# Optimization experiments

Hardware: AMD Instinct MI355X
Metric: run time of the kernel (lower is better)

Reference implementation:

```python
import jax, jax.numpy as jnp
import numpy as np

B, S, LQ = 32, 1024, 128
EMB = 256; H = 256; NH = 8; DH = H // NH
NCATE, NCONT, NNODE = 4, 8, 4
VOCAB = 50000
EPS = 1e-5
LK = S - LQ


def _ln(x, g, b):
    mu = jnp.mean(x, -1, keepdims=True)
    xc = x - mu
    var = jnp.mean(xc * xc, -1, keepdims=True)
    return xc * jax.lax.rsqrt(var + EPS) * g + b


def _leaky(x):
    return jnp.where(x >= 0, x, 0.01 * x)  # LeakyReLU slope 0.01 (torch default)


def setup_inputs() -> dict:
    key = jax.random.key(0)
    ks = jax.random.split(key, 48)
    rnd = lambda i, shape, scale=0.02: jax.random.normal(ks[i], shape, dtype=jnp.float32) * scale
    rng = np.random.default_rng(0)
    qidx = jnp.asarray(np.sort(rng.choice(S, LQ, replace=False)).astype(np.int64))
    cate_table = rnd(6, (VOCAB, EMB)).at[0].set(0.0)  # padding_idx=0
    inp = {
        "node": jax.random.normal(ks[0], (B, S, EMB * NNODE), dtype=jnp.float32),
        "cate": jax.random.randint(ks[1], (B, S, NCATE), 0, VOCAB),
        "cont": jax.random.normal(ks[2], (B, S, NCONT), dtype=jnp.float32),
        "query_index": qidx,
        "mask": jax.random.bernoulli(ks[3], 0.1, (B, LK)),
        "cate_table": cate_table,
        "pos_emb": rnd(4, (1, S, H)),
        "node_W": rnd(5, (EMB * NNODE, H)), "node_b": jnp.zeros((H,), jnp.float32),
        "node_ln_g": jnp.ones((H,), jnp.float32), "node_ln_b": jnp.zeros((H,), jnp.float32),
        "cate_W": rnd(7, (EMB * NCATE, H)), "cate_b": jnp.zeros((H,), jnp.float32),
        "cate_ln_g": jnp.ones((H,), jnp.float32), "cate_ln_b": jnp.zeros((H,), jnp.float32),
        "bn_g": jnp.ones((NCONT,), jnp.float32), "bn_b": jnp.zeros((NCONT,), jnp.float32),
        "cont_W": rnd(8, (NCONT, H)), "cont_b": jnp.zeros((H,), jnp.float32),
        "cont_ln_g": jnp.ones((H,), jnp.float32), "cont_ln_b": jnp.zeros((H,), jnp.float32),
        "comb_W": rnd(9, (3 * H, H)), "comb_b": jnp.zeros((H,), jnp.float32),
        "comb_ln_g": jnp.ones((H,), jnp.float32), "comb_ln_b": jnp.zeros((H,), jnp.float32),
        "q_W": rnd(10, (H, H)), "q_b": jnp.zeros((H,), jnp.float32),
        "k_W": rnd(11, (H, H)), "k_b": jnp.zeros((H,), jnp.float32),
        "v_W": rnd(12, (H, H)), "v_b": jnp.zeros((H,), jnp.float32),
        "reg_W1": rnd(13, (H, H)), "reg_b1": jnp.zeros((H,), jnp.float32),
        "reg_ln_g": jnp.ones((H,), jnp.float32), "reg_ln_b": jnp.zeros((H,), jnp.float32),
        "reg_W2": rnd(14, (H, H)), "reg_b2": jnp.zeros((H,), jnp.float32),
    }
    return inp


def reference(node, cate, cont, query_index, mask, cate_table, pos_emb,
              node_W, node_b, node_ln_g, node_ln_b,
              cate_W, cate_b, cate_ln_g, cate_ln_b,
              bn_g, bn_b, cont_W, cont_b, cont_ln_g, cont_ln_b,
              comb_W, comb_b, comb_ln_g, comb_ln_b,
              q_W, q_b, k_W, k_b, v_W, v_b,
              reg_W1, reg_b1, reg_ln_g, reg_ln_b, reg_W2, reg_b2):
    # --- three embedding branches: Linear -> LayerNorm ---
    node_e = _ln(node @ node_W + node_b, node_ln_g, node_ln_b)
    ce = cate_table[cate].reshape(B, S, NCATE * EMB)  # embedding gather
    cate_e = _ln(ce @ cate_W + cate_b, cate_ln_g, cate_ln_b)
    # BatchNorm1d (training-mode batch stats, biased var) over flattened [B*S, C]
    cf = cont.reshape(-1, NCONT)
    mu = jnp.mean(cf, 0)
    var = jnp.mean((cf - mu) ** 2, 0)
    cn = ((cf - mu) * jax.lax.rsqrt(var + EPS) * bn_g + bn_b).reshape(B, S, NCONT)
    cont_e = _ln(cn @ cont_W + cont_b, cont_ln_g, cont_ln_b)
    # --- combine + positions ---
    seq = jnp.concatenate([node_e, cate_e, cont_e], -1)       # [B,S,3H]
    seq = _ln(_leaky(seq) @ comb_W + comb_b, comb_ln_g, comb_ln_b) + pos_emb  # [B,S,H]
    # --- gather-split cross attention: queries vs complement keys ---
    is_q = jnp.zeros((S,), bool).at[query_index].set(True)
    key_index = jnp.nonzero(~is_q, size=LK)[0]                # setdiff1d, static size
    q = seq[:, query_index]                                   # [B,LQ,H]
    kv = seq[:, key_index]                                    # [B,LK,H]
    Q = (q @ q_W + q_b).reshape(B, LQ, NH, DH).transpose(0, 2, 1, 3)
    K = (kv @ k_W + k_b).reshape(B, LK, NH, DH).transpose(0, 2, 1, 3)
    V = (kv @ v_W + v_b).reshape(B, LK, NH, DH).transpose(0, 2, 1, 3)
    scale = jnp.float32(1.0 / np.sqrt(DH))
    scores = jnp.einsum('bhqd,bhkd->bhqk', Q, K) * scale      # [B,NH,LQ,LK]
    scores = jnp.where(mask[:, None, None, :], jnp.float32(-1e9), scores)
    attn = jax.nn.softmax(scores, -1)                         # dropout = identity (eval)
    out = jnp.einsum('bhqk,bhkd->bhqd', attn, V).transpose(0, 2, 1, 3).reshape(B, LQ, H)
    h = _leaky(_ln(out @ reg_W1 + reg_b1, reg_ln_g, reg_ln_b))
    return h @ reg_W2 + reg_b2                                # [B,LQ,H]
```

## Files before the change

### kernel.cpp

```cpp
#include <hip/hip_runtime.h>
#include <cstdint>

#define EPSV 1e-5f
#define AS1 __attribute__((address_space(1)))
#define AS3 __attribute__((address_space(3)))

typedef __attribute__((ext_vector_type(8))) short short8v;
typedef __attribute__((ext_vector_type(4))) float float4v;

__device__ inline unsigned short f2bf(float f) {
    union { float f; unsigned int u; } v; v.f = f;
    unsigned int r = v.u + 0x7FFF + ((v.u >> 16) & 1);
    return (unsigned short)(r >> 16);
}

__device__ inline size_t bidx(int n, int k) {
    return ((size_t)(k >> 5) << 13) + ((size_t)(n >> 4) << 9)
         + (((k >> 3) & 3) << 7) + ((n & 15) << 3) + (k & 7);
}

__device__ inline void issue_b(const unsigned short* Bc, int s, unsigned short* bsb,
                               int w, int l) {
    const unsigned short* g = Bc + ((size_t)s << 13) + (w << 9) + (l << 3);
    unsigned short* d = bsb + (w << 9) + (l << 3);
    #pragma unroll
    for (int i = 0; i < 4; ++i)
        __builtin_amdgcn_global_load_lds((const AS1 void*)(g + (i << 11)),
                                         (AS3 void*)(d + (i << 11)), 16, 0, 0);
}

__global__ __launch_bounds__(256) void wt_all_k(
    const float* __restrict__ nW, const float* __restrict__ cW, const float* __restrict__ mW,
    const float* __restrict__ qW, const float* __restrict__ kW, const float* __restrict__ vW,
    const float* __restrict__ r1W, const float* __restrict__ r2W,
    unsigned short* __restrict__ nO, unsigned short* __restrict__ cO, unsigned short* __restrict__ mO,
    unsigned short* __restrict__ qO, unsigned short* __restrict__ kO, unsigned short* __restrict__ vO,
    unsigned short* __restrict__ r1O, unsigned short* __restrict__ r2O)
{
    __shared__ float T[64][65];
    int bid = blockIdx.x;
    const float* W; unsigned short* O; int K, tile;
    if (bid < 64)       { W = nW; O = nO; K = 1024; tile = bid; }
    else if (bid < 128) { W = cW; O = cO; K = 1024; tile = bid - 64; }
    else if (bid < 176) { W = mW; O = mO; K = 768;  tile = bid - 128; }
    else {
        int s = (bid - 176) >> 4; tile = (bid - 176) & 15; K = 256;
        switch (s) {
            case 0: W = qW;  O = qO;  break;
            case 1: W = kW;  O = kO;  break;
            case 2: W = vW;  O = vO;  break;
            case 3: W = r1W; O = r1O; break;
            default: W = r2W; O = r2O; break;
        }
    }
    int kTiles = K >> 6;
    int k0 = (tile % kTiles) * 64, n0 = (tile / kTiles) * 64;
    int c = threadIdx.x & 63, r4 = threadIdx.x >> 6;
    #pragma unroll
    for (int rr = 0; rr < 64; rr += 4) {
        int r = rr + r4;
        T[r][c] = W[(size_t)(k0 + r) * 256 + n0 + c];
    }
    __syncthreads();
    #pragma unroll
    for (int rr = 0; rr < 64; rr += 4) {
        int n = rr + r4;
        O[bidx(n0 + n, k0 + c)] = f2bf(T[c][n]);
    }
}

__global__ __launch_bounds__(256) void gemm_nc_k(
    const float* __restrict__ node, const int* __restrict__ cate,
    const float* __restrict__ table,
    const unsigned short* __restrict__ nWt, const unsigned short* __restrict__ cWt,
    const float* __restrict__ nb, const float* __restrict__ cb,
    const float* __restrict__ nlg, const float* __restrict__ nlb,
    const float* __restrict__ clg, const float* __restrict__ clb,
    unsigned short* __restrict__ Y)
{
    __shared__ unsigned short As[2][64][40];
    __shared__ unsigned short Bs[2][8192];
    __shared__ float redS[64][4], redQ[64][4];
    const int t = threadIdx.x;
    const bool isC = blockIdx.x >= 512;
    const int bm = (isC ? (int)blockIdx.x - 512 : (int)blockIdx.x) * 64;
    const int w = t >> 6, l = t & 63, lr = l & 15, lg = l >> 4;
    const int arow = t >> 2, ac8 = (t & 3) * 8;

    const unsigned short* Bc = isC ? cWt : nWt;
    const float* bias = isC ? cb : nb;
    const float* lng  = isC ? clg : nlg;
    const float* lnbp = isC ? clb : nlb;
    const int colOff = isC ? 256 : 0;

    const float* apf = node + (size_t)(bm + arow) * 1024 + ac8;
    int4 idx4 = {0,0,0,0};
    if (isC) idx4 = *(const int4*)&cate[(bm + arow) * 4];

    float4v acc[4][4];
    #pragma unroll
    for (int i = 0; i < 4; ++i)
        #pragma unroll
        for (int j = 0; j < 4; ++j) acc[i][j] = (float4v)0.f;

    float4 fA0, fA1, fB0, fB1;

    auto loadA = [&](int s, float4& f0, float4& f1) {
        int kt = s * 32;
        const float* p;
        if (isC) {
            int g = kt >> 8;
            int idx = (g == 0) ? idx4.x : (g == 1) ? idx4.y : (g == 2) ? idx4.z : idx4.w;
            p = table + (size_t)idx * 256 + (kt & 255) + ac8;
        } else {
            p = apf + kt;
        }
        f0 = *(const float4*)p;
        f1 = *(const float4*)(p + 4);
    };
    auto writeA = [&](const float4& f0, const float4& f1, unsigned short (*Asb)[40]) {
        short8v av;
        av[0] = (short)f2bf(f0.x); av[1] = (short)f2bf(f0.y);
        av[2] = (short)f2bf(f0.z); av[3] = (short)f2bf(f0.w);
        av[4] = (short)f2bf(f1.x); av[5] = (short)f2bf(f1.y);
        av[6] = (short)f2bf(f1.z); av[7] = (short)f2bf(f1.w);
        *(short8v*)&Asb[arow][ac8] = av;
    };
    auto comp = [&](unsigned short (*Asb)[40], unsigned short* bsb) {
        short8v af[4], bf[4];
        #pragma unroll
        for (int i = 0; i < 4; ++i) af[i] = *(const short8v*)&Asb[i*16 + lr][lg*8];
        #pragma unroll
        for (int j = 0; j < 4; ++j)
            bf[j] = *(const short8v*)&bsb[((w*4 + j) << 9) + (lg << 7) + (lr << 3)];
        #pragma unroll
        for (int i = 0; i < 4; ++i)
            #pragma unroll
            for (int j = 0; j < 4; ++j)
                acc[i][j] = __builtin_amdgcn_mfma_f32_16x16x32_bf16(af[i], bf[j], acc[i][j], 0, 0, 0);
    };

    issue_b(Bc, 0, &Bs[0][0], w, l);
    loadA(0, fA0, fA1);
    for (int s = 0; s < 32; ++s) {
        int cur = s & 1;
        __syncthreads();
        writeA(fA0, fA1, As[cur]);
        __syncthreads();
        if (s + 1 < 32) {
            issue_b(Bc, s + 1, &Bs[1 - cur][0], w, l);
            loadA(s + 1, fB0, fB1);
        }
        comp(As[cur], &Bs[cur][0]);
        fA0 = fB0; fA1 = fB1;
    }

    float bv[4];
    #pragma unroll
    for (int j = 0; j < 4; ++j) bv[j] = bias[w*64 + j*16 + lr];
    #pragma unroll
    for (int i = 0; i < 4; ++i)
        #pragma unroll
        for (int j = 0; j < 4; ++j)
            #pragma unroll
            for (int r4 = 0; r4 < 4; ++r4) acc[i][j][r4] += bv[j];

    float ps[4][4], qs[4][4];
    #pragma unroll
    for (int i = 0; i < 4; ++i)
        #pragma unroll
        for (int r4 = 0; r4 < 4; ++r4) {
            float a0 = acc[i][0][r4], a1 = acc[i][1][r4],
                  a2 = acc[i][2][r4], a3 = acc[i][3][r4];
            ps[i][r4] = (a0 + a1) + (a2 + a3);
            qs[i][r4] = (a0*a0 + a1*a1) + (a2*a2 + a3*a3);
        }
    #pragma unroll
    for (int o = 1; o < 16; o <<= 1)
        #pragma unroll
        for (int i = 0; i < 4; ++i)
            #pragma unroll
            for (int r4 = 0; r4 < 4; ++r4) {
                ps[i][r4] += __shfl_xor(ps[i][r4], o);
                qs[i][r4] += __shfl_xor(qs[i][r4], o);
            }
    if (lr == 0) {
        #pragma unroll
        for (int i = 0; i < 4; ++i)
            #pragma unroll
            for (int r4 = 0; r4 < 4; ++r4) {
                redS[i*16 + lg*4 + r4][w] = ps[i][r4];
                redQ[i*16 + lg*4 + r4][w] = qs[i][r4];
            }
    }
    __syncthreads();
    #pragma unroll
    for (int i = 0; i < 4; ++i) {
        float mu[4], rstd[4];
        #pragma unroll
        for (int r4 = 0; r4 < 4; ++r4) {
            int rl = i*16 + lg*4 + r4;
            float s  = (redS[rl][0] + redS[rl][1]) + (redS[rl][2] + redS[rl][3]);
            float qq = (redQ[rl][0] + redQ[rl][1]) + (redQ[rl][2] + redQ[rl][3]);
            float m_ = s * (1.0f/256.0f);
            mu[r4] = m_;
            rstd[r4] = rsqrtf(qq * (1.0f/256.0f) - m_*m_ + EPSV);
        }
        #pragma unroll
        for (int j = 0; j < 4; ++j) {
            int c = w*64 + j*16 + lr;
            float gv = lng[c], b2 = lnbp[c];
            #pragma unroll
            for (int r4 = 0; r4 < 4; ++r4) {
                int row = bm + i*16 + lg*4 + r4;
                float y = (acc[i][j][r4] - mu[r4]) * rstd[r4] * gv + b2;
                y = (y >= 0.f) ? y : 0.01f*y;
                Y[(size_t)row * 768 + colOff + c] = f2bf(y);
            }
        }
    }
}

__global__ __launch_bounds__(256) void gemm_comb_k(
    const unsigned short* __restrict__ A,
    const unsigned short* __restrict__ Bc,
    const float* __restrict__ bias,
    const float* __restrict__ lng, const float* __restrict__ lnbp,
    const float* __restrict__ pos,
    unsigned short* __restrict__ Y)
{
    __shared__ unsigned short As[2][32][40];
    __shared__ unsigned short Bs[2][8192];
    __shared__ float redS[32][4], redQ[32][4];
    const int t = threadIdx.x;
    const int bm = blockIdx.x * 32;
    const int w = t >> 6, l = t & 63, lr = l & 15, lg = l >> 4;
    const int arow = (t & 127) >> 2;
    const int ac8  = (t & 3) * 8;
    const bool aLane = t < 128;

    const unsigned short* ap = A + (size_t)(bm + arow) * 768 + ac8;

    float4v acc[2][4];
    #pragma unroll
    for (int i = 0; i < 2; ++i)
        #pragma unroll
        for (int j = 0; j < 4; ++j) acc[i][j] = (float4v)0.f;

    short8v aA, aB;

    auto comp = [&](unsigned short (*Asb)[40], unsigned short* bsb) {
        short8v af[2], bf[4];
        #pragma unroll
        for (int i = 0; i < 2; ++i) af[i] = *(const short8v*)&Asb[i*16 + lr][lg*8];
        #pragma unroll
        for (int j = 0; j < 4; ++j)
            bf[j] = *(const short8v*)&bsb[((w*4 + j) << 9) + (lg << 7) + (lr << 3)];
        #pragma unroll
        for (int i = 0; i < 2; ++i)
            #pragma unroll
            for (int j = 0; j < 4; ++j)
                acc[i][j] = __builtin_amdgcn_mfma_f32_16x16x32_bf16(af[i], bf[j], acc[i][j], 0, 0, 0);
    };

    issue_b(Bc, 0, &Bs[0][0], w, l);
    if (aLane) aA = *(const short8v*)(ap);
    for (int s = 0; s < 24; ++s) {
        int cur = s & 1;
        __syncthreads();
        if (aLane) *(short8v*)&As[cur][arow][ac8] = aA;
        __syncthreads();
        if (s + 1 < 24) {
            issue_b(Bc, s + 1, &Bs[1 - cur][0], w, l);
            if (aLane) aB = *(const short8v*)(ap + (s + 1) * 32);
        }
        comp(As[cur], &Bs[cur][0]);
        aA = aB;
    }

    float bv[4];
    #pragma unroll
    for (int j = 0; j < 4; ++j) bv[j] = bias[w*64 + j*16 + lr];
    #pragma unroll
    for (int i = 0; i < 2; ++i)
        #pragma unroll
        for (int j = 0; j < 4; ++j)
            #pragma unroll
            for (int r4 = 0; r4 < 4; ++r4) acc[i][j][r4] += bv[j];

    float ps[2][4], qs[2][4];
    #pragma unroll
    for (int i = 0; i < 2; ++i)
        #pragma unroll
        for (int r4 = 0; r4 < 4; ++r4) {
            float a0 = acc[i][0][r4], a1 = acc[i][1][r4],
                  a2 = acc[i][2][r4], a3 = acc[i][3][r4];
            ps[i][r4] = (a0 + a1) + (a2 + a3);
            qs[i][r4] = (a0*a0 + a1*a1) + (a2*a2 + a3*a3);
        }
    #pragma unroll
    for (int o = 1; o < 16; o <<= 1)
        #pragma unroll
        for (int i = 0; i < 2; ++i)
            #pragma unroll
            for (int r4 = 0; r4 < 4; ++r4) {
                ps[i][r4] += __shfl_xor(ps[i][r4], o);
                qs[i][r4] += __shfl_xor(qs[i][r4], o);
            }
    if (lr == 0) {
        #pragma unroll
        for (int i = 0; i < 2; ++i)
            #pragma unroll
            for (int r4 = 0; r4 < 4; ++r4) {
                redS[i*16 + lg*4 + r4][w] = ps[i][r4];
                redQ[i*16 + lg*4 + r4][w] = qs[i][r4];
            }
    }
    __syncthreads();
    #pragma unroll
    for (int i = 0; i < 2; ++i) {
        float mu[4], rstd[4];
        #pragma unroll
        for (int r4 = 0; r4 < 4; ++r4) {
            int rl = i*16 + lg*4 + r4;
            float s  = (redS[rl][0] + redS[rl][1]) + (redS[rl][2] + redS[rl][3]);
            float qq = (redQ[rl][0] + redQ[rl][1]) + (redQ[rl][2] + redQ[rl][3]);
            float m_ = s * (1.0f/256.0f);
            mu[r4] = m_;
            rstd[r4] = rsqrtf(qq * (1.0f/256.0f) - m_*m_ + EPSV);
        }
        #pragma unroll
        for (int j = 0; j < 4; ++j) {
            int c = w*64 + j*16 + lr;
            float gv = lng[c], b2 = lnbp[c];
            #pragma unroll
            for (int r4 = 0; r4 < 4; ++r4) {
                int row = bm + i*16 + lg*4 + r4;
                float y = (acc[i][j][r4] - mu[r4]) * rstd[r4] * gv + b2
                        + pos[(size_t)(row & 1023) * 256 + c];
                Y[(size_t)row * 256 + c] = f2bf(y);
            }
        }
    }
}

__global__ __launch_bounds__(256) void gemm_qkv_k(
    const unsigned short* __restrict__ seq,
    const int* __restrict__ qmap, const int* __restrict__ krmap,
    const unsigned short* __restrict__ qWt, const unsigned short* __restrict__ kWt,
    const unsigned short* __restrict__ vWt,
    const float* __restrict__ qb, const float* __restrict__ kb, const float* __restrict__ vb,
    unsigned short* __restrict__ Qo, unsigned short* __restrict__ Ko,
    unsigned short* __restrict__ Vt)
{
    __shared__ unsigned short As[2][64][40];
    __shared__ unsigned short Bs[2][8192];
    const int t = threadIdx.x;
    const int bid = blockIdx.x;
    int seg, bm;
    const int* gmap; const unsigned short* Bc; const float* bias;
    if (bid < 64)       { seg = 0; bm = bid * 64;         gmap = qmap;  Bc = qWt; bias = qb; }
    else if (bid < 512) { seg = 1; bm = (bid - 64) * 64;  gmap = krmap; Bc = kWt; bias = kb; }
    else                { seg = 2; bm = (bid - 512) * 64; gmap = krmap; Bc = vWt; bias = vb; }
    const int w = t >> 6, l = t & 63, lr = l & 15, lg = l >> 4;
    const int arow = t >> 2, ac8 = (t & 3) * 8;

    const unsigned short* ap = seq + (size_t)gmap[bm + arow] * 256 + ac8;

    float4v acc[4][4];
    #pragma unroll
    for (int i = 0; i < 4; ++i)
        #pragma unroll
        for (int j = 0; j < 4; ++j) acc[i][j] = (float4v)0.f;

    short8v aA, aB;

    auto comp = [&](unsigned short (*Asb)[40], unsigned short* bsb) {
        short8v af[4], bf[4];
        #pragma unroll
        for (int i = 0; i < 4; ++i) af[i] = *(const short8v*)&Asb[i*16 + lr][lg*8];
        #pragma unroll
        for (int j = 0; j < 4; ++j)
            bf[j] = *(const short8v*)&bsb[((w*4 + j) << 9) + (lg << 7) + (lr << 3)];
        #pragma unroll
        for (int i = 0; i < 4; ++i)
            #pragma unroll
            for (int j = 0; j < 4; ++j)
                acc[i][j] = __builtin_amdgcn_mfma_f32_16x16x32_bf16(af[i], bf[j], acc[i][j], 0, 0, 0);
    };

    issue_b(Bc, 0, &Bs[0][0], w, l);
    aA = *(const short8v*)(ap);
    for (int s = 0; s < 8; ++s) {
        int cur = s & 1;
        __syncthreads();
        *(short8v*)&As[cur][arow][ac8] = aA;
        __syncthreads();
        if (s + 1 < 8) {
            issue_b(Bc, s + 1, &Bs[1 - cur][0], w, l);
            aB = *(const short8v*)(ap + (s + 1) * 32);
        }
        comp(As[cur], &Bs[cur][0]);
        aA = aB;
    }

    float bv[4];
    #pragma unroll
    for (int j = 0; j < 4; ++j) bv[j] = bias[w*64 + j*16 + lr];
    unsigned short* outp = (seg == 0) ? Qo : (seg == 1) ? Ko : Vt;
    #pragma unroll
    for (int i = 0; i < 4; ++i) {
        #pragma unroll
        for (int j = 0; j < 4; ++j) {
            int c = w*64 + j*16 + lr;
            #pragma unroll
            for (int r4 = 0; r4 < 4; ++r4) {
                int rl = i*16 + lg*4 + r4;
                float val = acc[i][j][r4] + bv[j];
                if (seg < 2) {
                    outp[(size_t)(bm + rl) * 256 + c] = f2bf(val);
                } else {
                    int vbk = bm / 896;
                    int kl = bm - vbk * 896 + rl;
                    outp[((size_t)vbk * 256 + c) * 896 + kl] = f2bf(val);
                }
            }
        }
    }
}

template<int EPI>
__global__ __launch_bounds__(256) void gemm_reg_k(
    const unsigned short* __restrict__ Asrc,
    const unsigned short* __restrict__ Bc,
    const float* __restrict__ bias,
    const float* __restrict__ ln_g,
    const float* __restrict__ ln_b,
    void* __restrict__ Cout)
{
    __shared__ unsigned short As[2][64][40];
    __shared__ unsigned short Bs[2][8192];
    __shared__ float redS[64][4], redQ[64][4];
    const int t = threadIdx.x;
    const int bm = blockIdx.x * 64;
    const int w = t >> 6, l = t & 63, lr = l & 15, lg = l >> 4;
    const int arow = t >> 2, ac8 = (t & 3) * 8;

    const unsigned short* ap = Asrc + (size_t)(bm + arow) * 256 + ac8;

    float4v acc[4][4];
    #pragma unroll
    for (int i = 0; i < 4; ++i)
        #pragma unroll
        for (int j = 0; j < 4; ++j) acc[i][j] = (float4v)0.f;

    short8v aA, aB;

    auto comp = [&](unsigned short (*Asb)[40], unsigned short* bsb) {
        short8v af[4], bf[4];
        #pragma unroll
        for (int i = 0; i < 4; ++i) af[i] = *(const short8v*)&Asb[i*16 + lr][lg*8];
        #pragma unroll
        for (int j = 0; j < 4; ++j)
            bf[j] = *(const short8v*)&bsb[((w*4 + j) << 9) + (lg << 7) + (lr << 3)];
        #pragma unroll
        for (int i = 0; i < 4; ++i)
            #pragma unroll
            for (int j = 0; j < 4; ++j)
                acc[i][j] = __builtin_amdgcn_mfma_f32_16x16x32_bf16(af[i], bf[j], acc[i][j], 0, 0, 0);
    };

    issue_b(Bc, 0, &Bs[0][0], w, l);
    aA = *(const short8v*)(ap);
    for (int s = 0; s < 8; ++s) {
        int cur = s & 1;
        __syncthreads();
        *(short8v*)&As[cur][arow][ac8] = aA;
        __syncthreads();
        if (s + 1 < 8) {
            issue_b(Bc, s + 1, &Bs[1 - cur][0], w, l);
            aB = *(const short8v*)(ap + (s + 1) * 32);
        }
        comp(As[cur], &Bs[cur][0]);
        aA = aB;
    }

    float bv[4];
    #pragma unroll
    for (int j = 0; j < 4; ++j) bv[j] = bias[w*64 + j*16 + lr];
    #pragma unroll
    for (int i = 0; i < 4; ++i)
        #pragma unroll
        for (int j = 0; j < 4; ++j)
            #pragma unroll
            for (int r4 = 0; r4 < 4; ++r4) acc[i][j][r4] += bv[j];

    if (EPI == 0) {
        #pragma unroll
        for (int i = 0; i < 4; ++i)
            #pragma unroll
            for (int j = 0; j < 4; ++j) {
                int c = w*64 + j*16 + lr;
                #pragma unroll
                for (int r4 = 0; r4 < 4; ++r4) {
                    int rl = i*16 + lg*4 + r4;
                    ((float*)Cout)[(size_t)(bm + rl) * 256 + c] = acc[i][j][r4];
                }
            }
    } else {
        float ps[4][4], qs[4][4];
        #pragma unroll
        for (int i = 0; i < 4; ++i)
            #pragma unroll
            for (int r4 = 0; r4 < 4; ++r4) {
                float a0 = acc[i][0][r4], a1 = acc[i][1][r4],
                      a2 = acc[i][2][r4], a3 = acc[i][3][r4];
                ps[i][r4] = (a0 + a1) + (a2 + a3);
                qs[i][r4] = (a0*a0 + a1*a1) + (a2*a2 + a3*a3);
            }
        #pragma unroll
        for (int o = 1; o < 16; o <<= 1)
            #pragma unroll
            for (int i = 0; i < 4; ++i)
                #pragma unroll
                for (int r4 = 0; r4 < 4; ++r4) {
                    ps[i][r4] += __shfl_xor(ps[i][r4], o);
                    qs[i][r4] += __shfl_xor(qs[i][r4], o);
                }
        if (lr == 0) {
            #pragma unroll
            for (int i = 0; i < 4; ++i)
                #pragma unroll
                for (int r4 = 0; r4 < 4; ++r4) {
                    redS[i*16 + lg*4 + r4][w] = ps[i][r4];
                    redQ[i*16 + lg*4 + r4][w] = qs[i][r4];
                }
        }
        __syncthreads();
        #pragma unroll
        for (int i = 0; i < 4; ++i) {
            float mu[4], rstd[4];
            #pragma unroll
            for (int r4 = 0; r4 < 4; ++r4) {
                int rl = i*16 + lg*4 + r4;
                float s  = (redS[rl][0] + redS[rl][1]) + (redS[rl][2] + redS[rl][3]);
                float qq = (redQ[rl][0] + redQ[rl][1]) + (redQ[rl][2] + redQ[rl][3]);
                float m_ = s * (1.0f/256.0f);
                mu[r4] = m_;
                rstd[r4] = rsqrtf(qq * (1.0f/256.0f) - m_*m_ + EPSV);
            }
            #pragma unroll
            for (int j = 0; j < 4; ++j) {
                int c = w*64 + j*16 + lr;
                float gv = ln_g[c], b2 = ln_b[c];
                #pragma unroll
                for (int r4 = 0; r4 < 4; ++r4) {
                    int row = bm + i*16 + lg*4 + r4;
                    float y = (acc[i][j][r4] - mu[r4]) * rstd[r4] * gv + b2;
                    y = (y >= 0.f) ? y : 0.01f*y;
                    ((unsigned short*)Cout)[(size_t)row * 256 + c] = f2bf(y);
                }
            }
        }
    }
}

__global__ __launch_bounds__(256) void bn_stats_k(const float* __restrict__ cont,
                                                  float* __restrict__ stats)
{
    __shared__ float ss[8], sq[8];
    int tid = threadIdx.x;
    if (tid < 8) { ss[tid] = 0.f; sq[tid] = 0.f; }
    __syncthreads();
    int gt = blockIdx.x * 256 + tid;
    float s = 0.f, q = 0.f;
    for (int e = gt; e < 32768*8; e += 256*256) { float v = cont[e]; s += v; q += v*v; }
    int f = gt & 7;
    atomicAdd(&ss[f], s);
    atomicAdd(&sq[f], q);
    __syncthreads();
    if (tid < 8) { atomicAdd(&stats[tid], ss[tid]); atomicAdd(&stats[8+tid], sq[tid]); }
}

__global__ __launch_bounds__(256) void cont_k(
    const float* __restrict__ cont, const float* __restrict__ stats,
    const float* __restrict__ bn_g, const float* __restrict__ bn_b,
    const float* __restrict__ W, const float* __restrict__ bias,
    const float* __restrict__ g, const float* __restrict__ bL,
    unsigned short* __restrict__ seq3)
{
    __shared__ float Ws[8][256];
    __shared__ float sscale[8], sshift[8];
    __shared__ float cr[8];
    __shared__ float red[8];
    int tid = threadIdx.x;
    #pragma unroll
    for (int d = 0; d < 8; ++d) Ws[d][tid] = W[d*256 + tid];
    if (tid < 8) {
        float mean = stats[tid] * (1.0f/32768.0f);
        float var  = stats[8+tid] * (1.0f/32768.0f) - mean*mean;
        float r = rsqrtf(var + EPSV);
        float sc = r * bn_g[tid];
        sscale[tid] = sc;
        sshift[tid] = bn_b[tid] - mean*sc;
    }
    __syncthreads();
    int lane = tid & 63, wv = tid >> 6;
    float gv = g[tid], bv = bL[tid], biasv = bias[tid];
    for (int row = blockIdx.x; row < 32768; row += gridDim.x) {
        if (tid < 8) cr[tid] = cont[(size_t)row*8 + tid]*sscale[tid] + sshift[tid];
        __syncthreads();
        float acc = biasv;
        #pragma unroll
        for (int d = 0; d < 8; ++d) acc += cr[d]*Ws[d][tid];
        float s = acc;
        #pragma unroll
        for (int o = 32; o; o >>= 1) s += __shfl_xor(s, o);
        if (lane == 0) red[wv] = s;
        __syncthreads();
        float mu = (red[0]+red[1]+red[2]+red[3]) * (1.0f/256.0f);
        float dc = acc - mu;
        float qv = dc*dc;
        #pragma unroll
        for (int o = 32; o; o >>= 1) qv += __shfl_xor(qv, o);
        if (lane == 0) red[4+wv] = qv;
        __syncthreads();
        float var = (red[4]+red[5]+red[6]+red[7]) * (1.0f/256.0f);
        float y = dc * rsqrtf(var + EPSV) * gv + bv;
        y = (y >= 0.f) ? y : 0.01f*y;
        seq3[(size_t)row*768 + 512 + tid] = f2bf(y);
        __syncthreads();
    }
}

__global__ void build_maps_k(const int* __restrict__ qidx, int* __restrict__ kmap)
{
    __shared__ int flag[1024];
    __shared__ int scan[1024];
    int t = threadIdx.x;
    flag[t] = 0;
    __syncthreads();
    if (t < 128) flag[qidx[t]] = 1;
    __syncthreads();
    int nq = 1 - flag[t];
    scan[t] = nq;
    __syncthreads();
    for (int off = 1; off < 1024; off <<= 1) {
        int v = (t >= off) ? scan[t - off] : 0;
        __syncthreads();
        scan[t] += v;
        __syncthreads();
    }
    if (nq) kmap[scan[t] - 1] = t;
}

__global__ void expand_maps_k(const int* __restrict__ qidx, const int* __restrict__ kmap,
                              int* __restrict__ qmap, int* __restrict__ krmap)
{
    int i = blockIdx.x * 256 + threadIdx.x;
    if (i < 32*128) { int b = i >> 7; int t = i & 127; qmap[i] = b*1024 + qidx[t]; }
    if (i < 32*896) { int b = i / 896; int t = i - b*896; krmap[i] = b*1024 + kmap[t]; }
}

__global__ __launch_bounds__(256) void mask_sniff_k(const unsigned char* __restrict__ msrc,
                                                    int* __restrict__ flags)
{
    int i = blockIdx.x * 256 + threadIdx.x;
    unsigned char v = msrc[i];
    bool u8  = v && (i & 3);
    bool i32 = v && !(i & 3) && ((i & 7) == 4);
    unsigned long long bu = __ballot(u8);
    unsigned long long bi = __ballot(i32);
    if ((threadIdx.x & 63) == 0) {
        if (bu) atomicOr(&flags[0], 1);
        if (bi) atomicOr(&flags[1], 1);
    }
}

__global__ __launch_bounds__(256) void mask_conv_k(const unsigned char* __restrict__ msrc,
                                                   const int* __restrict__ flags,
                                                   unsigned char* __restrict__ mu8)
{
    int i = blockIdx.x * 256 + threadIdx.x;
    int mode = flags[0] ? 0 : (flags[1] ? 1 : 2);
    unsigned char v;
    if (mode == 0)      v = msrc[i] ? 1 : 0;
    else if (mode == 1) v = ((const int*)msrc)[i] ? 1 : 0;
    else                v = ((const long long*)msrc)[i] ? 1 : 0;
    mu8[i] = v;
}

__global__ __launch_bounds__(256) void attn_mfma_k(
    const unsigned short* __restrict__ Qb,
    const unsigned short* __restrict__ Kb,
    const unsigned short* __restrict__ Vtb,
    const unsigned char* __restrict__ mask,
    unsigned short* __restrict__ out)
{
    __shared__ unsigned short Pw[4][16][72];
    const int t = threadIdx.x;
    const int w = t >> 6, l = t & 63;
    const int lr = l & 15, lg = l >> 4;
    const int bx = blockIdx.x;
    const int qh = bx & 1, h = (bx >> 1) & 7, b = bx >> 4;
    const int qrow0 = b*128 + qh*64 + w*16;

    short8v qf = *(const short8v*)&Qb[(size_t)(qrow0 + lr)*256 + h*32 + lg*8];

    const unsigned short* Kbase = Kb + (size_t)b*896*256 + h*32;
    const unsigned short* Vbase = Vtb + ((size_t)b*256 + h*32)*896;
    const unsigned char* mrow = mask + b*896;

    float4v O0 = (float4v)0.f, O1 = (float4v)0.f;
    float m[4], lsum[4];
    #pragma unroll
    for (int r = 0; r < 4; ++r) { m[r] = -3.0e38f; lsum[r] = 0.f; }

    short8v kf[4], vf[4];
    int mk[4];
    #pragma unroll
    for (int i = 0; i < 4; ++i) {
        kf[i] = *(const short8v*)&Kbase[(size_t)(i*16 + lr)*256 + lg*8];
        mk[i] = mrow[i*16 + lr];
    }
    #pragma unroll
    for (int kc = 0; kc < 2; ++kc)
        #pragma unroll
        for (int nt = 0; nt < 2; ++nt)
            vf[kc*2+nt] = *(const short8v*)&Vbase[(size_t)(nt*16 + lr)*896 + kc*32 + lg*8];

    for (int kt3 = 0; kt3 < 14; ++kt3) {
        const int kb2 = kt3*64 + 64;
        short8v kf2[4], vf2[4];
        int mk2[4];
        if (kt3 < 13) {
            #pragma unroll
            for (int i = 0; i < 4; ++i) {
                kf2[i] = *(const short8v*)&Kbase[(size_t)(kb2 + i*16 + lr)*256 + lg*8];
                mk2[i] = mrow[kb2 + i*16 + lr];
            }
            #pragma unroll
            for (int kc = 0; kc < 2; ++kc)
                #pragma unroll
                for (int nt = 0; nt < 2; ++nt)
                    vf2[kc*2+nt] = *(const short8v*)&Vbase[(size_t)(nt*16 + lr)*896 + kb2 + kc*32 + lg*8];
        }
        float4v s4[4];
        #pragma unroll
        for (int i = 0; i < 4; ++i)
            s4[i] = __builtin_amdgcn_mfma_f32_16x16x32_bf16(qf, kf[i], (float4v)0.f, 0, 0, 0);
        #pragma unroll
        for (int i = 0; i < 4; ++i)
            #pragma unroll
            for (int r = 0; r < 4; ++r)
                s4[i][r] = mk[i] ? -1e9f : s4[i][r] * 0.17677669529663687f;
        float tm[4];
        #pragma unroll
        for (int r = 0; r < 4; ++r)
            tm[r] = fmaxf(fmaxf(s4[0][r], s4[1][r]), fmaxf(s4[2][r], s4[3][r]));
        #pragma unroll
        for (int o = 1; o < 16; o <<= 1)
            #pragma unroll
            for (int r = 0; r < 4; ++r) tm[r] = fmaxf(tm[r], __shfl_xor(tm[r], o));
        float resc[4];
        #pragma unroll
        for (int r = 0; r < 4; ++r) {
            float mn = fmaxf(m[r], tm[r]);
            resc[r] = __expf(m[r] - mn);
            m[r] = mn;
        }
        float rs[4] = {0.f, 0.f, 0.f, 0.f};
        #pragma unroll
        for (int i = 0; i < 4; ++i)
            #pragma unroll
            for (int r = 0; r < 4; ++r) {
                float p = __expf(s4[i][r] - m[r]);
                s4[i][r] = p;
                rs[r] += p;
            }
        #pragma unroll
        for (int o = 1; o < 16; o <<= 1)
            #pragma unroll
            for (int r = 0; r < 4; ++r) rs[r] += __shfl_xor(rs[r], o);
        #pragma unroll
        for (int r = 0; r < 4; ++r) lsum[r] = lsum[r]*resc[r] + rs[r];
        #pragma unroll
        for (int r = 0; r < 4; ++r) { O0[r] *= resc[r]; O1[r] *= resc[r]; }
        #pragma unroll
        for (int i = 0; i < 4; ++i)
            #pragma unroll
            for (int r = 0; r < 4; ++r)
                Pw[w][lg*4 + r][i*16 + lr] = f2bf(s4[i][r]);
        #pragma unroll
        for (int kc = 0; kc < 2; ++kc) {
            short8v pf = *(const short8v*)&Pw[w][lr][kc*32 + lg*8];
            O0 = __builtin_amdgcn_mfma_f32_16x16x32_bf16(pf, vf[kc*2+0], O0, 0, 0, 0);
            O1 = __builtin_amdgcn_mfma_f32_16x16x32_bf16(pf, vf[kc*2+1], O1, 0, 0, 0);
        }
        if (kt3 < 13) {
            #pragma unroll
            for (int i = 0; i < 4; ++i) { kf[i] = kf2[i]; mk[i] = mk2[i]; vf[i] = vf2[i]; }
        }
    }
    #pragma unroll
    for (int r = 0; r < 4; ++r) {
        float inv = 1.0f / lsum[r];
        size_t row = (size_t)(qrow0 + lg*4 + r);
        out[row*256 + h*32 + lr]      = f2bf(O0[r] * inv);
        out[row*256 + h*32 + 16 + lr] = f2bf(O1[r] * inv);
    }
}

extern "C" void kernel_launch(void* const* d_in, const int* in_sizes, int n_in,
                              void* d_out, int out_size, void* d_ws, size_t ws_size,
                              hipStream_t stream)
{
    const float* node       = (const float*)d_in[0];
    const int*   cate       = (const int*)d_in[1];
    const float* cont       = (const float*)d_in[2];
    const int*   qidx       = (const int*)d_in[3];
    const unsigned char* mask = (const unsigned char*)d_in[4];
    const float* cate_table = (const float*)d_in[5];
    const float* pos_emb    = (const float*)d_in[6];
    const float* node_W     = (const float*)d_in[7];
    const float* node_b     = (const float*)d_in[8];
    const float* node_ln_g  = (const float*)d_in[9];
    const float* node_ln_b  = (const float*)d_in[10];
    const float* cate_W     = (const float*)d_in[11];
    const float* cate_b     = (const float*)d_in[12];
    const float* cate_ln_g  = (const float*)d_in[13];
    const float* cate_ln_b  = (const float*)d_in[14];
    const float* bn_g       = (const float*)d_in[15];
    const float* bn_b       = (const float*)d_in[16];
    const float* cont_W     = (const float*)d_in[17];
    const float* cont_b     = (const float*)d_in[18];
    const float* cont_ln_g  = (const float*)d_in[19];
    const float* cont_ln_b  = (const float*)d_in[20];
    const float* comb_W     = (const float*)d_in[21];
    const float* comb_b     = (const float*)d_in[22];
    const float* comb_ln_g  = (const float*)d_in[23];
    const float* comb_ln_b  = (const float*)d_in[24];
    const float* q_W        = (const float*)d_in[25];
    const float* q_b        = (const float*)d_in[26];
    const float* k_W        = (const float*)d_in[27];
    const float* k_b        = (const float*)d_in[28];
    const float* v_W        = (const float*)d_in[29];
    const float* v_b        = (const float*)d_in[30];
    const float* reg_W1     = (const float*)d_in[31];
    const float* reg_b1     = (const float*)d_in[32];
    const float* reg_ln_g   = (const float*)d_in[33];
    const float* reg_ln_b   = (const float*)d_in[34];
    const float* reg_W2     = (const float*)d_in[35];
    const float* reg_b2     = (const float*)d_in[36];

    char* ws = (char*)d_ws;
    unsigned short* seq3bf = (unsigned short*)(ws + 0);
    unsigned short* seqbf  = (unsigned short*)(ws + 83886080);
    unsigned short* Qbf    = (unsigned short*)(ws + 100663296);
    unsigned short* Kbf    = (unsigned short*)(ws + 102760448);
    unsigned short* Vtbf   = (unsigned short*)(ws + 117440512);
    unsigned short* AObf   = (unsigned short*)(ws + 132120576);
    unsigned short* Hbf    = (unsigned short*)(ws + 0);
    float* stats = (float*)(ws + 165675008);
    int*   flags = (int*)  (ws + 165675072);
    int*   kmap  = (int*)  (ws + 165675136);
    int*   qmap  = (int*)  (ws + 165678720);
    int*   krmap = (int*)  (ws + 165695104);
    unsigned char* mu8 = (unsigned char*)(ws + 165809792);
    unsigned short* node_Wt = (unsigned short*)(ws + 165838464);
    unsigned short* cate_Wt = (unsigned short*)(ws + 166362752);
    unsigned short* comb_Wt = (unsigned short*)(ws + 166887040);
    unsigned short* q_Wt    = (unsigned short*)(ws + 167280256);
    unsigned short* k_Wt    = (unsigned short*)(ws + 167411328);
    unsigned short* v_Wt    = (unsigned short*)(ws + 167542400);
    unsigned short* r1_Wt   = (unsigned short*)(ws + 167673472);
    unsigned short* r2_Wt   = (unsigned short*)(ws + 167804544);
    float* outp = (float*)d_out;

    hipMemsetAsync(stats, 0, 128, stream);
    bn_stats_k<<<256, 256, 0, stream>>>(cont, stats);
    mask_sniff_k<<<112, 256, 0, stream>>>(mask, flags);
    mask_conv_k<<<112, 256, 0, stream>>>(mask, flags, mu8);
    wt_all_k<<<256, 256, 0, stream>>>(node_W, cate_W, comb_W, q_W, k_W, v_W, reg_W1, reg_W2,
                                      node_Wt, cate_Wt, comb_Wt, q_Wt, k_Wt, v_Wt, r1_Wt, r2_Wt);

    gemm_nc_k<<<1024, 256, 0, stream>>>(node, cate, cate_table, node_Wt, cate_Wt,
        node_b, cate_b, node_ln_g, node_ln_b, cate_ln_g, cate_ln_b, seq3bf);
    cont_k<<<2048, 256, 0, stream>>>(cont, stats, bn_g, bn_b, cont_W, cont_b,
                                     cont_ln_g, cont_ln_b, seq3bf);
    gemm_comb_k<<<1024, 256, 0, stream>>>(seq3bf, comb_Wt, comb_b,
        comb_ln_g, comb_ln_b, pos_emb, seqbf);
    build_maps_k<<<1, 1024, 0, stream>>>(qidx, kmap);
    expand_maps_k<<<112, 256, 0, stream>>>(qidx, kmap, qmap, krmap);
    gemm_qkv_k<<<960, 256, 0, stream>>>(seqbf, qmap, krmap, q_Wt, k_Wt, v_Wt,
        q_b, k_b, v_b, Qbf, Kbf, Vtbf);
    attn_mfma_k<<<512, 256, 0, stream>>>(Qbf, Kbf, Vtbf, mu8, AObf);
    gemm_reg_k<3><<<64, 256, 0, stream>>>(AObf, r1_Wt, reg_b1, reg_ln_g, reg_ln_b, Hbf);
    gemm_reg_k<0><<<64, 256, 0, stream>>>(Hbf, r2_Wt, reg_b2, nullptr, nullptr, outp);
}
```

Before: 283.8 us.

## Pre-convert node and embedding table to bf16 and stream A tiles to LDS

A new prep kernel converts the whole node tensor and the whole categorical embedding table from fp32 to bf16 in workspace. All GEMM kernels then load A tiles with global_load_lds directly into unpadded shared buffers, instead of staging them through registers. This drops the register-to-LDS write and one __syncthreads per k-step. In exchange it adds a full extra pass over node and the table: it reads the fp32 data, writes bf16 and reads it back. The unpadded A layout may also cause LDS bank conflicts.

```diff
diff --git a/kernel.cpp b/kernel.cpp
--- a/kernel.cpp
+++ b/kernel.cpp
@@ -19,14 +19,35 @@
          + (((k >> 3) & 3) << 7) + ((n & 15) << 3) + (k & 7);
 }
 
+__device__ inline void gld16(const unsigned short* g, unsigned short* d) {
+    __builtin_amdgcn_global_load_lds((const AS1 void*)g, (AS3 void*)d, 16, 0, 0);
+}
+
 __device__ inline void issue_b(const unsigned short* Bc, int s, unsigned short* bsb,
                                int w, int l) {
     const unsigned short* g = Bc + ((size_t)s << 13) + (w << 9) + (l << 3);
     unsigned short* d = bsb + (w << 9) + (l << 3);
     #pragma unroll
     for (int i = 0; i < 4; ++i)
-        __builtin_amdgcn_global_load_lds((const AS1 void*)(g + (i << 11)),
-                                         (AS3 void*)(d + (i << 11)), 16, 0, 0);
+        gld16(g + (i << 11), d + (i << 11));
+}
+
+__global__ __launch_bounds__(256) void prep_k(
+    const float* __restrict__ node, const float* __restrict__ table,
+    unsigned short* __restrict__ nodebf, unsigned short* __restrict__ tabbf)
+{
+    size_t id = (size_t)blockIdx.x * 256 + threadIdx.x;
+    const float* src; unsigned short* dst; size_t e;
+    if (blockIdx.x < 16384) { e = id * 8; src = node; dst = nodebf; }
+    else { e = (id - (size_t)16384 * 256) * 8; src = table; dst = tabbf; }
+    float4 a = *(const float4*)(src + e);
+    float4 b = *(const float4*)(src + e + 4);
+    short8v v;
+    v[0] = (short)f2bf(a.x); v[1] = (short)f2bf(a.y);
+    v[2] = (short)f2bf(a.z); v[3] = (short)f2bf(a.w);
+    v[4] = (short)f2bf(b.x); v[5] = (short)f2bf(b.y);
+    v[6] = (short)f2bf(b.z); v[7] = (short)f2bf(b.w);
+    *(short8v*)(dst + e) = v;
 }
 
 __global__ __launch_bounds__(256) void wt_all_k(
@@ -70,22 +91,25 @@
 }
 
 __global__ __launch_bounds__(256) void gemm_nc_k(
-    const float* __restrict__ node, const int* __restrict__ cate,
-    const float* __restrict__ table,
+    const unsigned short* __restrict__ nodebf, const int* __restrict__ cate,
+    const unsigned short* __restrict__ tabbf,
     const unsigned short* __restrict__ nWt, const unsigned short* __restrict__ cWt,
     const float* __restrict__ nb, const float* __restrict__ cb,
     const float* __restrict__ nlg, const float* __restrict__ nlb,
     const float* __restrict__ clg, const float* __restrict__ clb,
     unsigned short* __restrict__ Y)
 {
-    __shared__ unsigned short As[2][64][40];
+    __shared__ union UN {
+        unsigned short A[2][2048];
+        struct { float S[64][4]; float Q[64][4]; } red;
+    } U;
     __shared__ unsigned short Bs[2][8192];
-    __shared__ float redS[64][4], redQ[64][4];
     const int t = threadIdx.x;
     const bool isC = blockIdx.x >= 512;
     const int bm = (isC ? (int)blockIdx.x - 512 : (int)blockIdx.x) * 64;
     const int w = t >> 6, l = t & 63, lr = l & 15, lg = l >> 4;
-    const int arow = t >> 2, ac8 = (t & 3) * 8;
+    const int ar = w*16 + (l >> 2);
+    const int ak = (l & 3) * 8;
 
     const unsigned short* Bc = isC ? cWt : nWt;
     const float* bias = isC ? cb : nb;
@@ -93,9 +117,10 @@
     const float* lnbp = isC ? clb : nlb;
     const int colOff = isC ? 256 : 0;
 
-    const float* apf = node + (size_t)(bm + arow) * 1024 + ac8;
+    const unsigned short* ap = nullptr;
     int4 idx4 = {0,0,0,0};
-    if (isC) idx4 = *(const int4*)&cate[(bm + arow) * 4];
+    if (isC) idx4 = *(const int4*)&cate[(bm + ar) * 4];
+    else     ap = nodebf + (size_t)(bm + ar) * 1024 + ak;
 
     float4v acc[4][4];
     #pragma unroll
@@ -103,33 +128,22 @@
         #pragma unroll
         for (int j = 0; j < 4; ++j) acc[i][j] = (float4v)0.f;
 
-    float4 fA0, fA1, fB0, fB1;
-
-    auto loadA = [&](int s, float4& f0, float4& f1) {
+    auto issueA = [&](int s, unsigned short* Ab) {
         int kt = s * 32;
-        const float* p;
+        const unsigned short* src;
         if (isC) {
             int g = kt >> 8;
             int idx = (g == 0) ? idx4.x : (g == 1) ? idx4.y : (g == 2) ? idx4.z : idx4.w;
-            p = table + (size_t)idx * 256 + (kt & 255) + ac8;
+            src = tabbf + (size_t)idx * 256 + (kt & 255) + ak;
         } else {
-            p = apf + kt;
-        }
-        f0 = *(const float4*)p;
-        f1 = *(const float4*)(p + 4);
+            src = ap + kt;
+        }
+        gld16(src, Ab + t * 8);
     };
-    auto writeA = [&](const float4& f0, const float4& f1, unsigned short (*Asb)[40]) {
-        short8v av;
-        av[0] = (short)f2bf(f0.x); av[1] = (short)f2bf(f0.y);
-        av[2] = (short)f2bf(f0.z); av[3] = (short)f2bf(f0.w);
-        av[4] = (short)f2bf(f1.x); av[5] = (short)f2bf(f1.y);
-        av[6] = (short)f2bf(f1.z); av[7] = (short)f2bf(f1.w);
-        *(short8v*)&Asb[arow][ac8] = av;
-    };
-    auto comp = [&](unsigned short (*Asb)[40], unsigned short* bsb) {
+    auto comp = [&](const unsigned short* Ab, const unsigned short* bsb) {
         short8v af[4], bf[4];
         #pragma unroll
-        for (int i = 0; i < 4; ++i) af[i] = *(const short8v*)&Asb[i*16 + lr][lg*8];
+        for (int i = 0; i < 4; ++i) af[i] = *(const short8v*)&Ab[(i*16 + lr)*32 + lg*8];
         #pragma unroll
         for (int j = 0; j < 4; ++j)
             bf[j] = *(const short8v*)&bsb[((w*4 + j) << 9) + (lg << 7) + (lr << 3)];
@@ -140,19 +154,16 @@
                 acc[i][j] = __builtin_amdgcn_mfma_f32_16x16x32_bf16(af[i], bf[j], acc[i][j], 0, 0, 0);
     };
 
+    issueA(0, U.A[0]);
     issue_b(Bc, 0, &Bs[0][0], w, l);
-    loadA(0, fA0, fA1);
     for (int s = 0; s < 32; ++s) {
         int cur = s & 1;
         __syncthreads();
-        writeA(fA0, fA1, As[cur]);
-        __syncthreads();
         if (s + 1 < 32) {
+            issueA(s + 1, U.A[1 - cur]);
             issue_b(Bc, s + 1, &Bs[1 - cur][0], w, l);
-            loadA(s + 1, fB0, fB1);
-        }
-        comp(As[cur], &Bs[cur][0]);
-        fA0 = fB0; fA1 = fB1;
+        }
+        comp(U.A[cur], &Bs[cur][0]);
     }
 
     float bv[4];
@@ -184,13 +195,14 @@
                 ps[i][r4] += __shfl_xor(ps[i][r4], o);
                 qs[i][r4] += __shfl_xor(qs[i][r4], o);
             }
+    __syncthreads();
     if (lr == 0) {
         #pragma unroll
         for (int i = 0; i < 4; ++i)
             #pragma unroll
             for (int r4 = 0; r4 < 4; ++r4) {
-                redS[i*16 + lg*4 + r4][w] = ps[i][r4];
-                redQ[i*16 + lg*4 + r4][w] = qs[i][r4];
+                U.red.S[i*16 + lg*4 + r4][w] = ps[i][r4];
+                U.red.Q[i*16 + lg*4 + r4][w] = qs[i][r4];
             }
     }
     __syncthreads();
@@ -200,8 +212,8 @@
         #pragma unroll
         for (int r4 = 0; r4 < 4; ++r4) {
             int rl = i*16 + lg*4 + r4;
-            float s  = (redS[rl][0] + redS[rl][1]) + (redS[rl][2] + redS[rl][3]);
-            float qq = (redQ[rl][0] + redQ[rl][1]) + (redQ[rl][2] + redQ[rl][3]);
+            float s  = (U.red.S[rl][0] + U.red.S[rl][1]) + (U.red.S[rl][2] + U.red.S[rl][3]);
+            float qq = (U.red.Q[rl][0] + U.red.Q[rl][1]) + (U.red.Q[rl][2] + U.red.Q[rl][3]);
             float m_ = s * (1.0f/256.0f);
             mu[r4] = m_;
             rstd[r4] = rsqrtf(qq * (1.0f/256.0f) - m_*m_ + EPSV);
@@ -229,17 +241,17 @@
     const float* __restrict__ pos,
     unsigned short* __restrict__ Y)
 {
-    __shared__ unsigned short As[2][32][40];
+    __shared__ union UC {
+        unsigned short A[2][1024];
+        struct { float S[32][4]; float Q[32][4]; } red;
+    } U;
     __shared__ unsigned short Bs[2][8192];
-    __shared__ float redS[32][4], redQ[32][4];
     const int t = threadIdx.x;
     const int bm = blockIdx.x * 32;
     const int w = t >> 6, l = t & 63, lr = l & 15, lg = l >> 4;
-    const int arow = (t & 127) >> 2;
-    const int ac8  = (t & 3) * 8;
     const bool aLane = t < 128;
 
-    const unsigned short* ap = A + (size_t)(bm + arow) * 768 + ac8;
+    const unsigned short* ap = A + (size_t)(bm + (t >> 2)) * 768 + (t & 3) * 8;
 
     float4v acc[2][4];
     #pragma unroll
@@ -247,12 +259,13 @@
         #pragma unroll
         for (int j = 0; j < 4; ++j) acc[i][j] = (float4v)0.f;
 
-    short8v aA, aB;
-
-    auto comp = [&](unsigned short (*Asb)[40], unsigned short* bsb) {
+    auto issueA = [&](int s, unsigned short* Ab) {
+        if (aLane) gld16(ap + s * 32, Ab + t * 8);
+    };
+    auto comp = [&](const unsigned short* Ab, const unsigned short* bsb) {
         short8v af[2], bf[4];
         #pragma unroll
-        for (int i = 0; i < 2; ++i) af[i] = *(const short8v*)&Asb[i*16 + lr][lg*8];
+        for (int i = 0; i < 2; ++i) af[i] = *(const short8v*)&Ab[(i*16 + lr)*32 + lg*8];
         #pragma unroll
         for (int j = 0; j < 4; ++j)
             bf[j] = *(const short8v*)&bsb[((w*4 + j) << 9) + (lg << 7) + (lr << 3)];
@@ -263,19 +276,16 @@
                 acc[i][j] = __builtin_amdgcn_mfma_f32_16x16x32_bf16(af[i], bf[j], acc[i][j], 0, 0, 0);
     };
 
+    issueA(0, U.A[0]);
     issue_b(Bc, 0, &Bs[0][0], w, l);
-    if (aLane) aA = *(const short8v*)(ap);
     for (int s = 0; s < 24; ++s) {
         int cur = s & 1;
         __syncthreads();
-        if (aLane) *(short8v*)&As[cur][arow][ac8] = aA;
-        __syncthreads();
         if (s + 1 < 24) {
+            issueA(s + 1, U.A[1 - cur]);
             issue_b(Bc, s + 1, &Bs[1 - cur][0], w, l);
-            if (aLane) aB = *(const short8v*)(ap + (s + 1) * 32);
-        }
-        comp(As[cur], &Bs[cur][0]);
-        aA = aB;
+        }
+        comp(U.A[cur], &Bs[cur][0]);
     }
 
     float bv[4];
@@ -307,13 +317,14 @@
                 ps[i][r4] += __shfl_xor(ps[i][r4], o);
                 qs[i][r4] += __shfl_xor(qs[i][r4], o);
             }
+    __syncthreads();
     if (lr == 0) {
         #pragma unroll
         for (int i = 0; i < 2; ++i)
             #pragma unroll
             for (int r4 = 0; r4 < 4; ++r4) {
-                redS[i*16 + lg*4 + r4][w] = ps[i][r4];
-                redQ[i*16 + lg*4 + r4][w] = qs[i][r4];
+                U.red.S[i*16 + lg*4 + r4][w] = ps[i][r4];
+                U.red.Q[i*16 + lg*4 + r4][w] = qs[i][r4];
             }
     }
     __syncthreads();
@@ -323,8 +334,8 @@
         #pragma unroll
         for (int r4 = 0; r4 < 4; ++r4) {
             int rl = i*16 + lg*4 + r4;
-            float s  = (redS[rl][0] + redS[rl][1]) + (redS[rl][2] + redS[rl][3]);
-            float qq = (redQ[rl][0] + redQ[rl][1]) + (redQ[rl][2] + redQ[rl][3]);
+            float s  = (U.red.S[rl][0] + U.red.S[rl][1]) + (U.red.S[rl][2] + U.red.S[rl][3]);
+            float qq = (U.red.Q[rl][0] + U.red.Q[rl][1]) + (U.red.Q[rl][2] + U.red.Q[rl][3]);
             float m_ = s * (1.0f/256.0f);
             mu[r4] = m_;
             rstd[r4] = rsqrtf(qq * (1.0f/256.0f) - m_*m_ + EPSV);
@@ -353,7 +364,7 @@
     unsigned short* __restrict__ Qo, unsigned short* __restrict__ Ko,
     unsigned short* __restrict__ Vt)
 {
-    __shared__ unsigned short As[2][64][40];
+    __shared__ unsigned short Asl[2][2048];
     __shared__ unsigned short Bs[2][8192];
     const int t = threadIdx.x;
     const int bid = blockIdx.x;
@@ -363,9 +374,9 @@
     else if (bid < 512) { seg = 1; bm = (bid - 64) * 64;  gmap = krmap; Bc = kWt; bias = kb; }
     else                { seg = 2; bm = (bid - 512) * 64; gmap = krmap; Bc = vWt; bias = vb; }
     const int w = t >> 6, l = t & 63, lr = l & 15, lg = l >> 4;
-    const int arow = t >> 2, ac8 = (t & 3) * 8;
-
-    const unsigned short* ap = seq + (size_t)gmap[bm + arow] * 256 + ac8;
+    const int ar = w*16 + (l >> 2), ak = (l & 3) * 8;
+
+    const unsigned short* ap = seq + (size_t)gmap[bm + ar] * 256 + ak;
 
     float4v acc[4][4];
     #pragma unroll
@@ -373,12 +384,10 @@
         #pragma unroll
         for (int j = 0; j < 4; ++j) acc[i][j] = (float4v)0.f;
 
-    short8v aA, aB;
-
-    auto comp = [&](unsigned short (*Asb)[40], unsigned short* bsb) {
+    auto comp = [&](const unsigned short* Ab, const unsigned short* bsb) {
         short8v af[4], bf[4];
         #pragma unroll
-        for (int i = 0; i < 4; ++i) af[i] = *(const short8v*)&Asb[i*16 + lr][lg*8];
+        for (int i = 0; i < 4; ++i) af[i] = *(const short8v*)&Ab[(i*16 + lr)*32 + lg*8];
         #pragma unroll
         for (int j = 0; j < 4; ++j)
             bf[j] = *(const short8v*)&bsb[((w*4 + j) << 9) + (lg << 7) + (lr << 3)];
@@ -389,19 +398,16 @@
                 acc[i][j] = __builtin_amdgcn_mfma_f32_16x16x32_bf16(af[i], bf[j], acc[i][j], 0, 0, 0);
     };
 
+    gld16(ap, Asl[0] + t * 8);
     issue_b(Bc, 0, &Bs[0][0], w, l);
-    aA = *(const short8v*)(ap);
     for (int s = 0; s < 8; ++s) {
         int cur = s & 1;
         __syncthreads();
-        *(short8v*)&As[cur][arow][ac8] = aA;
-        __syncthreads();
         if (s + 1 < 8) {
+            gld16(ap + (s + 1) * 32, Asl[1 - cur] + t * 8);
             issue_b(Bc, s + 1, &Bs[1 - cur][0], w, l);
-            aB = *(const short8v*)(ap + (s + 1) * 32);
-        }
-        comp(As[cur], &Bs[cur][0]);
-        aA = aB;
+        }
+        comp(Asl[cur], &Bs[cur][0]);
     }
 
     float bv[4];
@@ -438,15 +444,17 @@
     const float* __restrict__ ln_b,
     void* __restrict__ Cout)
 {
-    __shared__ unsigned short As[2][64][40];
+    __shared__ union UR {
+        unsigned short A[2][2048];
+        struct { float S[64][4]; float Q[64][4]; } red;
+    } U;
     __shared__ unsigned short Bs[2][8192];
-    __shared__ float redS[64][4], redQ[64][4];
     const int t = threadIdx.x;
     const int bm = blockIdx.x * 64;
     const int w = t >> 6, l = t & 63, lr = l & 15, lg = l >> 4;
-    const int arow = t >> 2, ac8 = (t & 3) * 8;
-
-    const unsigned short* ap = Asrc + (size_t)(bm + arow) * 256 + ac8;
+    const int ar = w*16 + (l >> 2), ak = (l & 3) * 8;
+
+    const unsigned short* ap = Asrc + (size_t)(bm + ar) * 256 + ak;
 
     float4v acc[4][4];
     #pragma unroll
@@ -454,12 +462,10 @@
         #pragma unroll
         for (int j = 0; j < 4; ++j) acc[i][j] = (float4v)0.f;
 
-    short8v aA, aB;
-
-    auto comp = [&](unsigned short (*Asb)[40], unsigned short* bsb) {
+    auto comp = [&](const unsigned short* Ab, const unsigned short* bsb) {
         short8v af[4], bf[4];
         #pragma unroll
-        for (int i = 0; i < 4; ++i) af[i] = *(const short8v*)&Asb[i*16 + lr][lg*8];
+        for (int i = 0; i < 4; ++i) af[i] = *(const short8v*)&Ab[(i*16 + lr)*32 + lg*8];
         #pragma unroll
         for (int j = 0; j < 4; ++j)
             bf[j] = *(const short8v*)&bsb[((w*4 + j) << 9) + (lg << 7) + (lr << 3)];
@@ -470,19 +476,16 @@
                 acc[i][j] = __builtin_amdgcn_mfma_f32_16x16x32_bf16(af[i], bf[j], acc[i][j], 0, 0, 0);
     };
 
+    gld16(ap, U.A[0] + t * 8);
     issue_b(Bc, 0, &Bs[0][0], w, l);
-    aA = *(const short8v*)(ap);
     for (int s = 0; s < 8; ++s) {
         int cur = s & 1;
         __syncthreads();
-        *(short8v*)&As[cur][arow][ac8] = aA;
-        __syncthreads();
         if (s + 1 < 8) {
+            gld16(ap + (s + 1) * 32, U.A[1 - cur] + t * 8);
             issue_b(Bc, s + 1, &Bs[1 - cur][0], w, l);
-            aB = *(const short8v*)(ap + (s + 1) * 32);
-        }
-        comp(As[cur], &Bs[cur][0]);
-        aA = aB;
+        }
+        comp(U.A[cur], &Bs[cur][0]);
     }
 
     float bv[4];
@@ -527,13 +530,14 @@
                     ps[i][r4] += __shfl_xor(ps[i][r4], o);
                     qs[i][r4] += __shfl_xor(qs[i][r4], o);
                 }
+        __syncthreads();
         if (lr == 0) {
             #pragma unroll
             for (int i = 0; i < 4; ++i)
                 #pragma unroll
                 for (int r4 = 0; r4 < 4; ++r4) {
-                    redS[i*16 + lg*4 + r4][w] = ps[i][r4];
-                    redQ[i*16 + lg*4 + r4][w] = qs[i][r4];
+                    U.red.S[i*16 + lg*4 + r4][w] = ps[i][r4];
+                    U.red.Q[i*16 + lg*4 + r4][w] = qs[i][r4];
                 }
         }
         __syncthreads();
@@ -543,8 +547,8 @@
             #pragma unroll
             for (int r4 = 0; r4 < 4; ++r4) {
                 int rl = i*16 + lg*4 + r4;
-                float s  = (redS[rl][0] + redS[rl][1]) + (redS[rl][2] + redS[rl][3]);
-                float qq = (redQ[rl][0] + redQ[rl][1]) + (redQ[rl][2] + redQ[rl][3]);
+                float s  = (U.red.S[rl][0] + U.red.S[rl][1]) + (U.red.S[rl][2] + U.red.S[rl][3]);
+                float qq = (U.red.Q[rl][0] + U.red.Q[rl][1]) + (U.red.Q[rl][2] + U.red.Q[rl][3]);
                 float m_ = s * (1.0f/256.0f);
                 mu[r4] = m_;
                 rstd[r4] = rsqrtf(qq * (1.0f/256.0f) - m_*m_ + EPSV);
@@ -855,11 +859,13 @@
 
     char* ws = (char*)d_ws;
     unsigned short* seq3bf = (unsigned short*)(ws + 0);
+    unsigned short* nodebf = (unsigned short*)(ws + 50331648);
     unsigned short* seqbf  = (unsigned short*)(ws + 83886080);
     unsigned short* Qbf    = (unsigned short*)(ws + 100663296);
     unsigned short* Kbf    = (unsigned short*)(ws + 102760448);
     unsigned short* Vtbf   = (unsigned short*)(ws + 117440512);
     unsigned short* AObf   = (unsigned short*)(ws + 132120576);
+    unsigned short* tabbf  = (unsigned short*)(ws + 134217728);
     unsigned short* Hbf    = (unsigned short*)(ws + 0);
     float* stats = (float*)(ws + 165675008);
     int*   flags = (int*)  (ws + 165675072);
@@ -883,8 +889,9 @@
     mask_conv_k<<<112, 256, 0, stream>>>(mask, flags, mu8);
     wt_all_k<<<256, 256, 0, stream>>>(node_W, cate_W, comb_W, q_W, k_W, v_W, reg_W1, reg_W2,
                                       node_Wt, cate_Wt, comb_Wt, q_Wt, k_Wt, v_Wt, r1_Wt, r2_Wt);
-
-    gemm_nc_k<<<1024, 256, 0, stream>>>(node, cate, cate_table, node_Wt, cate_Wt,
+    prep_k<<<22634, 256, 0, stream>>>(node, cate_table, nodebf, tabbf);
+
+    gemm_nc_k<<<1024, 256, 0, stream>>>(nodebf, cate, tabbf, node_Wt, cate_Wt,
         node_b, cate_b, node_ln_g, node_ln_b, cate_ln_g, cate_ln_b, seq3bf);
     cont_k<<<2048, 256, 0, stream>>>(cont, stats, bn_g, bn_b, cont_W, cont_b,
                                      cont_ln_g, cont_ln_b, seq3bf);
```

Result: slower. 341.9 us (+20.5%).
